# Kernel tuning notes

Measured on AMD Instinct MI355X. Metric: run time of the kernel, lower is better.

## Reference

```python
import jax, jax.numpy as jnp
import numpy as np

B, N1, N2, D, E = 8, 1024, 256, 16, 16


def setup_inputs() -> dict:
    key = jax.random.key(0)
    ks = jax.random.split(key, 11)
    stdv = 1.0 / np.sqrt(E)
    u = lambda k, shape: jax.random.uniform(k, shape, jnp.float32, -stdv, stdv)
    inputs = jax.random.normal(ks[0], (B, N1, N2, D), dtype=jnp.float32)
    # adjacency matrices (dense, nonnegative); scaled for numerical sanity
    adj0 = jax.random.uniform(ks[1], (N1, N1), dtype=jnp.float32) / np.float32(np.sqrt(N1))
    adj1 = jax.random.uniform(ks[2], (N2, N2), dtype=jnp.float32) / np.float32(np.sqrt(N2))
    return {
        "inputs": inputs, "adj0": adj0, "adj1": adj1,
        "W": u(ks[3], (D, E)), "b": u(ks[4], (E,)),
        "W_s0": u(ks[5], (D, E)), "b_s0": u(ks[6], (E,)),
        "W_s1": u(ks[7], (D, E)), "b_s1": u(ks[8], (E,)),
        "W_s01": u(ks[9], (D, E)), "b_s01": u(ks[10], (E,)),
    }


def _helper(x, adj_modes, W, b):
    # TGCNHelper: mode-wise adjacency products along the given tensor modes,
    # then a linear projection on the feature axis.
    h = x
    for mode, A in adj_modes:
        if mode == 0:
            h = jnp.einsum('bijd,ik->bkjd', h, A)  # mode-0 (n1) aggregation
        else:
            h = jnp.einsum('bijd,jk->bikd', h, A)  # mode-1 (n2) aggregation
    return jnp.einsum('bijd,de->bije', h, W) + b


def reference(inputs, adj0, adj1, W, b, W_s0, b_s0, W_s1, b_s1, W_s01, b_s01):
    # dense mode-product branch: inputs x_{-1} W + bias
    h_lin = jnp.einsum('bijd,de->bije', inputs, W) + b
    # subsets of valid_modes [0,1]: {0}, {1}, {0,1}
    h0 = _helper(inputs, [(0, adj0)], W_s0, b_s0)
    h1 = _helper(inputs, [(1, adj1)], W_s1, b_s1)
    h01 = _helper(inputs, [(0, adj0), (1, adj1)], W_s01, b_s01)
    # stack + sum over last dim == direct sum; then ReLU
    return jax.nn.relu(h_lin + h0 + h1 + h01)
```

## Files before the change

kernel.cpp:

```cpp
#include <hip/hip_runtime.h>

#define BB  8
#define NN1 1024
#define NN2 256
#define DD  16
#define EE  16
#define NCOL (NN2 * DD)
#define SLPB 2

using bf16x8  = __attribute__((ext_vector_type(8))) short;
using f32x4   = __attribute__((ext_vector_type(4))) float;
using ushort8 = __attribute__((ext_vector_type(8))) unsigned short;

__device__ __forceinline__ ushort f2bf(float x) {
  unsigned u = __float_as_uint(x);
  unsigned r = (u + 0x7FFFu + ((u >> 16) & 1u)) >> 16;
  return (ushort)r;
}
__device__ __forceinline__ float bf2f(ushort u) {
  return __uint_as_float((unsigned)u << 16);
}
__device__ __forceinline__ unsigned pkbf(float a, float b) {
  return (unsigned)f2bf(a) | ((unsigned)f2bf(b) << 16);
}

#define GLDS16(g, l)                                                       \
  __builtin_amdgcn_global_load_lds(                                        \
      (const __attribute__((address_space(1))) void*)(g),                  \
      (__attribute__((address_space(3))) void*)(l), 16, 0, 0)

__global__ __launch_bounds__(256)
void k_prep(const float* __restrict__ src, ushort* __restrict__ dst,
            int nr, int kd, size_t srcBatch, size_t dstBatch) {
  __shared__ float tile[64][65];
  const int t = threadIdx.x;
  const int r0 = blockIdx.x * 64;
  const int k0 = blockIdx.y * 64;
  const float* s = src + (size_t)blockIdx.z * srcBatch;
  ushort* d = dst + (size_t)blockIdx.z * dstBatch;

#pragma unroll
  for (int it = 0; it < 4; ++it) {
    const int kr = it * 16 + (t >> 4);
    const int rc = (t & 15) * 4;
    float4 v = *reinterpret_cast<const float4*>(&s[(size_t)(k0 + kr) * nr + r0 + rc]);
    tile[kr][rc] = v.x; tile[kr][rc + 1] = v.y;
    tile[kr][rc + 2] = v.z; tile[kr][rc + 3] = v.w;
  }
  __syncthreads();

#pragma unroll
  for (int pass = 0; pass < 2; ++pass) {
    const int task = t + pass * 256;
    const int pr = task >> 3;
    const int gl = task & 7;
    const int r = r0 + pr;
    const int f = (r >> 1) & 3;
    const int klb = (gl >> 2) * 32 + ((gl & 3) ^ f) * 8;
    unsigned w[4];
#pragma unroll
    for (int e2 = 0; e2 < 4; ++e2)
      w[e2] = pkbf(tile[klb + e2 * 2][pr], tile[klb + e2 * 2 + 1][pr]);
    *reinterpret_cast<uint4*>(&d[(size_t)r * kd + k0 + gl * 8]) =
        *reinterpret_cast<const uint4*>(w);
  }
}

__global__ __launch_bounds__(256)
void k_mode0_mfma(const ushort* __restrict__ At, const ushort* __restrict__ Xt,
                  ushort* __restrict__ Y) {
  __shared__ ushort As[2][4096];
  __shared__ ushort Bs[2][4096];

  const int t = threadIdx.x;
  const int lane = t & 63;
  const int wid = t >> 6;
  const int wm = wid >> 1, wn = wid & 1;
  const int b  = blockIdx.x >> 5;
  const int c0 = (blockIdx.x & 31) << 7;
  const int p0 = blockIdx.y << 7;

  const ushort* Bb = Xt + (size_t)b * (NCOL * 1024);

  f32x4 acc[4][4];
#pragma unroll
  for (int i = 0; i < 4; ++i)
#pragma unroll
    for (int j = 0; j < 4; ++j) acc[i][j] = (f32x4)0.f;

  const int srow = wid * 32 + (lane >> 2);
  const int schk = (lane & 3) * 8;
  const size_t aoff0 = (size_t)(p0 + srow) * 1024 + schk;
  const size_t boff0 = (size_t)(c0 + srow) * 1024 + schk;
  const int lw0 = (wid * 32) * 32;
  const int lw1 = (wid * 32 + 16) * 32;

  const int lm = lane & 15, g = lane >> 4;
  int aro[4], bro[4];
#pragma unroll
  for (int f = 0; f < 4; ++f) {
    const int ra = wm * 64 + f * 16 + lm;
    aro[f] = ra * 32 + ((g ^ ((ra >> 1) & 3)) << 3);
    const int rw = wn * 64 + f * 16 + lm;
    bro[f] = rw * 32 + ((g ^ ((rw >> 1) & 3)) << 3);
  }

#define STAGE0(buf, kk)                                                    \
  do {                                                                     \
    GLDS16(At + aoff0 + (kk), &As[buf][lw0]);                              \
    GLDS16(At + aoff0 + 16 * 1024 + (kk), &As[buf][lw1]);                  \
    GLDS16(Bb + boff0 + (kk), &Bs[buf][lw0]);                              \
    GLDS16(Bb + boff0 + 16 * 1024 + (kk), &Bs[buf][lw1]);                  \
  } while (0)

  STAGE0(0, 0);
  int cur = 0;

  for (int k0 = 0; k0 < 1024; k0 += 32) {
    if (k0 + 32 < 1024) {
      STAGE0(cur ^ 1, k0 + 32);
      asm volatile("s_waitcnt vmcnt(4)" ::: "memory");
    } else {
      asm volatile("s_waitcnt vmcnt(0)" ::: "memory");
    }
    __builtin_amdgcn_s_barrier();
    __builtin_amdgcn_sched_barrier(0);

    bf16x8 af[4], bfr[4];
#pragma unroll
    for (int f = 0; f < 4; ++f)
      af[f] = *reinterpret_cast<const bf16x8*>(&As[cur][aro[f]]);
#pragma unroll
    for (int f = 0; f < 4; ++f)
      bfr[f] = *reinterpret_cast<const bf16x8*>(&Bs[cur][bro[f]]);

#pragma unroll
    for (int i = 0; i < 4; ++i)
#pragma unroll
      for (int j = 0; j < 4; ++j)
        acc[i][j] = __builtin_amdgcn_mfma_f32_16x16x32_bf16(af[i], bfr[j], acc[i][j], 0, 0, 0);

    __builtin_amdgcn_sched_barrier(0);
    __builtin_amdgcn_s_barrier();
    cur ^= 1;
  }
#undef STAGE0

  ushort* Yb = Y + (size_t)b * (NN1 * NCOL);
  const int orow = g * 4;
  const int ocol = lm;
#pragma unroll
  for (int i = 0; i < 4; ++i)
#pragma unroll
    for (int j = 0; j < 4; ++j) {
      const int p = p0 + wm * 64 + i * 16 + orow;
      const int c = c0 + wn * 64 + j * 16 + ocol;
      ushort* dst = Yb + (size_t)p * NCOL + c;
#pragma unroll
      for (int e = 0; e < 4; ++e) dst[(size_t)e * NCOL] = f2bf(acc[i][j][e]);
    }
}

__global__ __launch_bounds__(512)
void k_pm(const float* __restrict__ x, const ushort* __restrict__ y0,
          const ushort* __restrict__ A1t,
          const float* __restrict__ W,   const float* __restrict__ bW,
          const float* __restrict__ W0,  const float* __restrict__ b0,
          const float* __restrict__ W1,  const float* __restrict__ b1,
          const float* __restrict__ W01, const float* __restrict__ b01,
          float* __restrict__ out) {
  __shared__ float sW[4][DD][EE];
  __shared__ float sbias[EE];
  __shared__ ushort St[8][SLPB * 16][32];
  __shared__ ushort Rb[SLPB][256][24];
  __shared__ ushort As[2][256 * 32];

  const int t = threadIdx.x;
  const int lane = t & 63;
  const int wid = t >> 6;
  const size_t sl0 = (size_t)blockIdx.x * SLPB;

  const int srow = wid * 32 + (lane >> 2);
  const int schk = (lane & 3) * 8;

#define STAGEA(buf, kc)                                                    \
  do {                                                                     \
    GLDS16(A1t + (size_t)srow * 256 + (kc) * 32 + schk,                    \
           &As[buf][(wid * 32) * 32]);                                     \
    GLDS16(A1t + (size_t)(srow + 16) * 256 + (kc) * 32 + schk,             \
           &As[buf][(wid * 32 + 16) * 32]);                                \
  } while (0)

  STAGEA(0, 0);

  {
    const int m = t >> 6;
    const int r = t & 63;
    if (t < 256) {
      const float* Wp = (m == 0) ? W : (m == 1) ? W0 : (m == 2) ? W1 : W01;
      reinterpret_cast<float4*>(&sW[m][0][0])[r] =
          reinterpret_cast<const float4*>(Wp)[r];
    }
    if (t < EE) sbias[t] = bW[t] + b0[t] + b1[t] + b01[t];
  }

  const int sl = t >> 8;
  const int j  = t & 255;
  const size_t base = (sl0 + sl) * NCOL + (size_t)j * DD;

  float xr[DD], yr[DD];
#pragma unroll
  for (int v = 0; v < 4; ++v)
    *reinterpret_cast<float4*>(&xr[v * 4]) =
        *reinterpret_cast<const float4*>(&x[base + v * 4]);
  {
    ushort8 ya = *reinterpret_cast<const ushort8*>(&y0[base]);
    ushort8 yb = *reinterpret_cast<const ushort8*>(&y0[base + 8]);
#pragma unroll
    for (int k = 0; k < 8; ++k) { yr[k] = bf2f(ya[k]); yr[8 + k] = bf2f(yb[k]); }
  }

  __syncthreads();

  float r[EE], s[EE];
#pragma unroll
  for (int e = 0; e < EE; ++e) { r[e] = sbias[e]; s[e] = 0.f; }

#pragma unroll
  for (int d = 0; d < DD; ++d) {
    const float xd = xr[d], yd = yr[d];
#pragma unroll
    for (int e = 0; e < EE; ++e) {
      r[e] = fmaf(xd, sW[0][d][e], r[e]);
      r[e] = fmaf(yd, sW[1][d][e], r[e]);
      s[e] = fmaf(xd, sW[2][d][e], s[e]);
      s[e] = fmaf(yd, sW[3][d][e], s[e]);
    }
  }

  {
    ushort rw[16];
#pragma unroll
    for (int e = 0; e < EE; ++e) rw[e] = f2bf(r[e]);
    *reinterpret_cast<uint4*>(&Rb[sl][j][0]) = *reinterpret_cast<const uint4*>(&rw[0]);
    *reinterpret_cast<uint4*>(&Rb[sl][j][8]) = *reinterpret_cast<const uint4*>(&rw[8]);
  }

  {
    const int kc = j >> 5;
    const int jj = j & 31;
#pragma unroll
    for (int e = 0; e < EE; ++e) {
      const int m = sl * 16 + e;
      const int idx = (((jj >> 3) ^ ((m >> 1) & 3)) << 3) + (jj & 7);
      St[kc][m][idx] = f2bf(s[e]);
    }
  }

  __syncthreads();

  const int lm = lane & 15, g = lane >> 4;
  const int wq  = wid >> 1;
  const int wmi = wid & 1;

  int aro[4];
#pragma unroll
  for (int f = 0; f < 4; ++f) {
    const int ra = wq * 64 + f * 16 + lm;
    aro[f] = ra * 32 + ((g ^ ((ra >> 1) & 3)) << 3);
  }
  const int rwB = wmi * 16 + lm;
  const int bofs = (rwB * 32) + ((g ^ ((rwB >> 1) & 3)) << 3);

  f32x4 acc[4];
#pragma unroll
  for (int i = 0; i < 4; ++i) acc[i] = (f32x4)0.f;

  int cur = 0;
  for (int kc = 0; kc < 8; ++kc) {
    if (kc < 7) {
      STAGEA(cur ^ 1, kc + 1);
      asm volatile("s_waitcnt vmcnt(2)" ::: "memory");
    } else {
      asm volatile("s_waitcnt vmcnt(0)" ::: "memory");
    }
    __builtin_amdgcn_s_barrier();
    __builtin_amdgcn_sched_barrier(0);

    bf16x8 af[4];
#pragma unroll
    for (int f = 0; f < 4; ++f)
      af[f] = *reinterpret_cast<const bf16x8*>(&As[cur][aro[f]]);
    const bf16x8 bfr = *reinterpret_cast<const bf16x8*>(&St[kc][0][0] + bofs);

#pragma unroll
    for (int i = 0; i < 4; ++i)
      acc[i] = __builtin_amdgcn_mfma_f32_16x16x32_bf16(af[i], bfr, acc[i], 0, 0, 0);

    __builtin_amdgcn_sched_barrier(0);
    __builtin_amdgcn_s_barrier();
    cur ^= 1;
  }
#undef STAGEA

  float* os = out + (sl0 + wmi) * NCOL;
#pragma unroll
  for (int i = 0; i < 4; ++i) {
    const int qb = wq * 64 + i * 16 + g * 4;
#pragma unroll
    for (int rr = 0; rr < 4; ++rr) {
      const int q = qb + rr;
      os[(size_t)q * EE + lm] =
          fmaxf(bf2f(Rb[wmi][q][lm]) + acc[i][rr], 0.f);
    }
  }
}

extern "C" void kernel_launch(void* const* d_in, const int* in_sizes, int n_in,
                              void* d_out, int out_size, void* d_ws, size_t ws_size,
                              hipStream_t stream) {
  const float* x    = (const float*)d_in[0];
  const float* adj0 = (const float*)d_in[1];
  const float* adj1 = (const float*)d_in[2];
  const float* W    = (const float*)d_in[3];
  const float* bW   = (const float*)d_in[4];
  const float* Ws0  = (const float*)d_in[5];
  const float* bs0  = (const float*)d_in[6];
  const float* Ws1  = (const float*)d_in[7];
  const float* bs1  = (const float*)d_in[8];
  const float* Ws01 = (const float*)d_in[9];
  const float* bs01 = (const float*)d_in[10];
  float* out = (float*)d_out;

  const size_t SLICE = (size_t)NN1 * NCOL;
  const size_t AT_B  = (size_t)1024 * 1024 * 2;
  const size_t A1T_B = (size_t)256 * 256 * 2;
  const size_t XT_B  = (size_t)NCOL * 1024 * 2;
  const size_t Y0_B  = SLICE * 2;
  const size_t HEAD  = AT_B + A1T_B;
  const size_t PER_B = XT_B + Y0_B;

  int nb_max = (int)((ws_size > HEAD ? ws_size - HEAD : 0) / PER_B);
  if (nb_max > BB) nb_max = BB;
  if (nb_max < 1)  nb_max = 1;

  ushort* At  = (ushort*)d_ws;
  ushort* A1t = (ushort*)((char*)d_ws + AT_B);
  ushort* Xt  = (ushort*)((char*)d_ws + HEAD);
  ushort* y0  = (ushort*)((char*)d_ws + HEAD + (size_t)nb_max * XT_B);

  k_prep<<<dim3(16, 16, 1), 256, 0, stream>>>(adj0, At, 1024, 1024, 0, 0);
  k_prep<<<dim3(4, 4, 1), 256, 0, stream>>>(adj1, A1t, 256, 256, 0, 0);

  for (int c0 = 0; c0 < BB; c0 += nb_max) {
    const int nb = (BB - c0 < nb_max) ? (BB - c0) : nb_max;
    const float* xc = x   + (size_t)c0 * SLICE;
    float*       oc = out + (size_t)c0 * SLICE;

    k_prep<<<dim3(NCOL / 64, 16, nb), 256, 0, stream>>>(
        xc, Xt, NCOL, 1024, SLICE, (size_t)NCOL * 1024);

    dim3 g1(nb * 32, 8);
    k_mode0_mfma<<<g1, 256, 0, stream>>>(At, Xt, y0);

    dim3 g2(nb * NN1 / SLPB);
    k_pm<<<g2, 512, 0, stream>>>(xc, y0, A1t, W, bW, Ws0, bs0,
                                 Ws1, bs1, Ws01, bs01, oc);
  }
}
```

Measured before the change: 236.8 us.

## Compute per-position feature projections with MFMA instead of scalar FMAs

The projection of x and the mode-0 aggregate y0 through the four weight matrices, previously done with 1024 scalar FMAs per thread, now uses bf16 MFMA. Inputs are staged in LDS as bf16 and the weights are packed into MFMA B fragments. The direct-path result now initialises the accumulator of the mode-1 GEMM, which removes the Rb shared buffer and the bf16 round-trip in the epilogue. In exchange, x is rounded to bf16 before the projection, which could cost some precision.

```diff
diff --git a/kernel.cpp b/kernel.cpp
--- a/kernel.cpp
+++ b/kernel.cpp
@@ -169,16 +169,71 @@
           const float* __restrict__ W1,  const float* __restrict__ b1,
           const float* __restrict__ W01, const float* __restrict__ b01,
           float* __restrict__ out) {
-  __shared__ float sW[4][DD][EE];
-  __shared__ float sbias[EE];
+  __shared__ ushort As[2][8192];
   __shared__ ushort St[8][SLPB * 16][32];
-  __shared__ ushort Rb[SLPB][256][24];
-  __shared__ ushort As[2][256 * 32];
 
   const int t = threadIdx.x;
   const int lane = t & 63;
   const int wid = t >> 6;
+  const int lm = lane & 15, g = lane >> 4;
+  const int wq  = wid >> 1;
+  const int wmi = wid & 1;
   const size_t sl0 = (size_t)blockIdx.x * SLPB;
+
+  {
+    const size_t base = (sl0 * NCOL) + (size_t)t * DD;
+    const float4 x0 = *reinterpret_cast<const float4*>(&x[base]);
+    const float4 x1 = *reinterpret_cast<const float4*>(&x[base + 4]);
+    const float4 x2 = *reinterpret_cast<const float4*>(&x[base + 8]);
+    const float4 x3 = *reinterpret_cast<const float4*>(&x[base + 12]);
+    const uint4 yv0 = *reinterpret_cast<const uint4*>(&y0[base]);
+    const uint4 yv1 = *reinterpret_cast<const uint4*>(&y0[base + 8]);
+    unsigned xw0[4] = {pkbf(x0.x, x0.y), pkbf(x0.z, x0.w), pkbf(x1.x, x1.y), pkbf(x1.z, x1.w)};
+    unsigned xw1[4] = {pkbf(x2.x, x2.y), pkbf(x2.z, x2.w), pkbf(x3.x, x3.y), pkbf(x3.z, x3.w)};
+    *reinterpret_cast<uint4*>(&As[0][t * 16])     = *reinterpret_cast<const uint4*>(xw0);
+    *reinterpret_cast<uint4*>(&As[0][t * 16 + 8]) = *reinterpret_cast<const uint4*>(xw1);
+    *reinterpret_cast<uint4*>(&As[1][t * 16])     = yv0;
+    *reinterpret_cast<uint4*>(&As[1][t * 16 + 8]) = yv1;
+  }
+
+  bf16x8 wfr, wfs;
+#pragma unroll
+  for (int jj = 0; jj < 8; ++jj) {
+    const int k = g * 8 + jj;
+    const float vr = (k < 16) ? W[k * 16 + lm]  : W0[(k - 16) * 16 + lm];
+    const float vs = (k < 16) ? W1[k * 16 + lm] : W01[(k - 16) * 16 + lm];
+    wfr[jj] = (short)f2bf(vr);
+    wfs[jj] = (short)f2bf(vs);
+  }
+  const float bias = bW[lm] + b0[lm] + b1[lm] + b01[lm];
+
+  __syncthreads();
+
+  f32x4 acc[4];
+#pragma unroll
+  for (int i = 0; i < 4; ++i) {
+    const int grp = wmi * 16 + wq * 4 + i;
+    const int row = grp * 16 + lm;
+    bf16x8 a;
+    if (g < 2)
+      a = *reinterpret_cast<const bf16x8*>(&As[0][row * 16 + g * 8]);
+    else
+      a = *reinterpret_cast<const bf16x8*>(&As[1][row * 16 + (g - 2) * 8]);
+
+    f32x4 cb; cb[0] = bias; cb[1] = bias; cb[2] = bias; cb[3] = bias;
+    acc[i] = __builtin_amdgcn_mfma_f32_16x16x32_bf16(a, wfr, cb, 0, 0, 0);
+    const f32x4 sD = __builtin_amdgcn_mfma_f32_16x16x32_bf16(a, wfs, (f32x4)0.f, 0, 0, 0);
+
+    const int m = wmi * 16 + lm;
+    const int kc = wq * 2 + (i >> 1);
+    const int chunkL = ((i & 1) << 1) + (g >> 1);
+    const int phys = chunkL ^ ((m >> 1) & 3);
+    unsigned pw[2] = {pkbf(sD[0], sD[1]), pkbf(sD[2], sD[3])};
+    *reinterpret_cast<uint2*>(&St[kc][m][phys * 8 + (g & 1) * 4]) =
+        *reinterpret_cast<const uint2*>(pw);
+  }
+
+  __syncthreads();
 
   const int srow = wid * 32 + (lane >> 2);
   const int schk = (lane & 3) * 8;
@@ -191,78 +246,6 @@
            &As[buf][(wid * 32 + 16) * 32]);                                \
   } while (0)
 
-  STAGEA(0, 0);
-
-  {
-    const int m = t >> 6;
-    const int r = t & 63;
-    if (t < 256) {
-      const float* Wp = (m == 0) ? W : (m == 1) ? W0 : (m == 2) ? W1 : W01;
-      reinterpret_cast<float4*>(&sW[m][0][0])[r] =
-          reinterpret_cast<const float4*>(Wp)[r];
-    }
-    if (t < EE) sbias[t] = bW[t] + b0[t] + b1[t] + b01[t];
-  }
-
-  const int sl = t >> 8;
-  const int j  = t & 255;
-  const size_t base = (sl0 + sl) * NCOL + (size_t)j * DD;
-
-  float xr[DD], yr[DD];
-#pragma unroll
-  for (int v = 0; v < 4; ++v)
-    *reinterpret_cast<float4*>(&xr[v * 4]) =
-        *reinterpret_cast<const float4*>(&x[base + v * 4]);
-  {
-    ushort8 ya = *reinterpret_cast<const ushort8*>(&y0[base]);
-    ushort8 yb = *reinterpret_cast<const ushort8*>(&y0[base + 8]);
-#pragma unroll
-    for (int k = 0; k < 8; ++k) { yr[k] = bf2f(ya[k]); yr[8 + k] = bf2f(yb[k]); }
-  }
-
-  __syncthreads();
-
-  float r[EE], s[EE];
-#pragma unroll
-  for (int e = 0; e < EE; ++e) { r[e] = sbias[e]; s[e] = 0.f; }
-
-#pragma unroll
-  for (int d = 0; d < DD; ++d) {
-    const float xd = xr[d], yd = yr[d];
-#pragma unroll
-    for (int e = 0; e < EE; ++e) {
-      r[e] = fmaf(xd, sW[0][d][e], r[e]);
-      r[e] = fmaf(yd, sW[1][d][e], r[e]);
-      s[e] = fmaf(xd, sW[2][d][e], s[e]);
-      s[e] = fmaf(yd, sW[3][d][e], s[e]);
-    }
-  }
-
-  {
-    ushort rw[16];
-#pragma unroll
-    for (int e = 0; e < EE; ++e) rw[e] = f2bf(r[e]);
-    *reinterpret_cast<uint4*>(&Rb[sl][j][0]) = *reinterpret_cast<const uint4*>(&rw[0]);
-    *reinterpret_cast<uint4*>(&Rb[sl][j][8]) = *reinterpret_cast<const uint4*>(&rw[8]);
-  }
-
-  {
-    const int kc = j >> 5;
-    const int jj = j & 31;
-#pragma unroll
-    for (int e = 0; e < EE; ++e) {
-      const int m = sl * 16 + e;
-      const int idx = (((jj >> 3) ^ ((m >> 1) & 3)) << 3) + (jj & 7);
-      St[kc][m][idx] = f2bf(s[e]);
-    }
-  }
-
-  __syncthreads();
-
-  const int lm = lane & 15, g = lane >> 4;
-  const int wq  = wid >> 1;
-  const int wmi = wid & 1;
-
   int aro[4];
 #pragma unroll
   for (int f = 0; f < 4; ++f) {
@@ -272,10 +255,7 @@
   const int rwB = wmi * 16 + lm;
   const int bofs = (rwB * 32) + ((g ^ ((rwB >> 1) & 3)) << 3);
 
-  f32x4 acc[4];
-#pragma unroll
-  for (int i = 0; i < 4; ++i) acc[i] = (f32x4)0.f;
-
+  STAGEA(0, 0);
   int cur = 0;
   for (int kc = 0; kc < 8; ++kc) {
     if (kc < 7) {
@@ -308,11 +288,8 @@
   for (int i = 0; i < 4; ++i) {
     const int qb = wq * 64 + i * 16 + g * 4;
 #pragma unroll
-    for (int rr = 0; rr < 4; ++rr) {
-      const int q = qb + rr;
-      os[(size_t)q * EE + lm] =
-          fmaxf(bf2f(Rb[wmi][q][lm]) + acc[i][rr], 0.f);
-    }
+    for (int rr = 0; rr < 4; ++rr)
+      os[(size_t)(qb + rr) * EE + lm] = fmaxf(acc[i][rr], 0.f);
   }
 }
 
```

After: 208.0 us. -12.2%, faster.
